# Kernel optimization log

Hardware: AMD Instinct MI355X
Metric: run time of the kernel (lower is better)

## Reference

```python
import jax, jax.numpy as jnp
import numpy as np
jax.config.update('jax_enable_x64', True)  # log_normalization accumulates in fp64 like the torch code

B = 256
N = 36864  # SO(3) HEALPix-style grid, level 3
EPS_TRACE = 1e-8


def quat_to_mat(q):
    # (w, x, y, z) convention; normalize to a unit quaternion first.
    q = q / jnp.linalg.norm(q, axis=-1, keepdims=True)
    w, x, y, z = q[..., 0], q[..., 1], q[..., 2], q[..., 3]
    return jnp.stack([
        jnp.stack([1 - 2 * (y * y + z * z), 2 * (x * y - w * z), 2 * (x * z + w * y)], -1),
        jnp.stack([2 * (x * y + w * z), 1 - 2 * (x * x + z * z), 2 * (y * z - w * x)], -1),
        jnp.stack([2 * (x * z - w * y), 2 * (y * z + w * x), 1 - 2 * (x * x + y * y)], -1),
    ], -2)


def cholesky_inverse(L):
    # (L L^T)^{-1} = L^{-T} L^{-1}; batched 3x3, inv is cheap and exact here.
    Linv = jnp.linalg.inv(L)
    return jnp.einsum('...ki,...kj->...ij', Linv, Linv)


def setup_inputs() -> dict:
    key = jax.random.key(0)
    k1, k2, k3, k4 = jax.random.split(key, 4)
    gt_quat = jax.random.normal(k1, (B, 4), dtype=jnp.float32)
    mode_quat = jax.random.normal(k2, (B, 4), dtype=jnp.float32)
    raw = jax.random.normal(k3, (B, 3, 3), dtype=jnp.float32)
    diag_vals = 0.3 + jax.nn.softplus(jnp.diagonal(raw, axis1=-2, axis2=-1))
    cov_tril = jnp.tril(raw, -1) * 0.2 + jnp.eye(3, dtype=jnp.float32) * diag_vals[:, None, :]
    grid_q = jax.random.normal(k4, (N, 4), dtype=jnp.float32)
    grids = quat_to_mat(grid_q)  # [N, 3, 3] rotation matrices
    return {'gt_quat': gt_quat, 'mode_quat': mode_quat, 'cov_tril': cov_tril, 'grids': grids}


def reference(gt_quat, mode_quat, cov_tril, grids):
    Z = cholesky_inverse(cov_tril)                      # [B,3,3] precision
    trZ = jnp.einsum('bii->b', Z)                       # tr(Z)

    # power over the grid: sqrt(clamp(tr(Z) - tr(Z @ R_n), eps)) for every grid rotation
    tr_ZR_grid = jnp.einsum('bij,nji->bn', Z, grids)    # [B,N] = diag-sum of Z @ R_n
    powers = jnp.sqrt(jnp.clip(trZ[:, None] - tr_ZR_grid, EPS_TRACE))  # [B,N] fp32

    # stable log-normalization (fp64 accumulation, as in the torch code)
    stability = jnp.min(powers, axis=-1)                # [B]
    p64 = powers.astype(jnp.float64)
    log_exp_sum = jnp.log(jnp.sum(jnp.exp(-p64 + stability[:, None].astype(jnp.float64)) / p64,
                                  axis=1)).astype(jnp.float32)
    logF = log_exp_sum - jnp.log(jnp.float32(N)) - stability

    # power at the ground truth relative rotation R = R0^T R_gt
    R_gt = quat_to_mat(gt_quat)
    R0 = quat_to_mat(mode_quat)
    R_rel = jnp.einsum('bki,bkj->bij', R0, R_gt)        # R0^T @ R_gt
    tr_ZR = jnp.einsum('bij,bji->b', Z, R_rel)
    power = jnp.sqrt(jnp.clip(trZ - tr_ZR, EPS_TRACE))  # [B]

    nll = logF + power + jnp.log(power)
    return nll
```

## Files before the change

kernel.cpp:

```cpp
#include <hip/hip_runtime.h>
#include <math.h>

#define TPB 256
#define KROT 6
#define BPB 8
#define NCHUNK (TPB * KROT)

__device__ __forceinline__ void compute_Z_neg(const float* __restrict__ L, float zo[7]) {
    float a = L[0], l10 = L[3], c = L[4], d = L[6], e = L[7], f = L[8];
    float ia = 1.0f / a, ic = 1.0f / c, iff = 1.0f / f;
    float m00 = ia;
    float m10 = -l10 * ia * ic;
    float m11 = ic;
    float m20 = (l10 * e - c * d) * ia * ic * iff;
    float m21 = -e * ic * iff;
    float m22 = iff;
    float Z0 = m00*m00 + m10*m10 + m20*m20;
    float Z1 = m10*m11 + m20*m21;
    float Z2 = m20*m22;
    float Z4 = m11*m11 + m21*m21;
    float Z5 = m21*m22;
    float Z8 = m22*m22;
    zo[0] = -Z0; zo[1] = -Z4; zo[2] = -Z8;
    zo[3] = -Z1; zo[4] = -Z2; zo[5] = -Z5;
    zo[6] = Z0 + Z4 + Z8;
}

__device__ __forceinline__ void quat_to_mat(const float q[4], float R[9]) {
    float n = sqrtf(q[0]*q[0] + q[1]*q[1] + q[2]*q[2] + q[3]*q[3]);
    float w = q[0]/n, x = q[1]/n, y = q[2]/n, z = q[3]/n;
    R[0] = 1.f - 2.f*(y*y + z*z);
    R[1] = 2.f*(x*y - w*z);
    R[2] = 2.f*(x*z + w*y);
    R[3] = 2.f*(x*y + w*z);
    R[4] = 1.f - 2.f*(x*x + z*z);
    R[5] = 2.f*(y*z - w*x);
    R[6] = 2.f*(x*z - w*y);
    R[7] = 2.f*(y*z + w*x);
    R[8] = 1.f - 2.f*(x*x + y*y);
}

__global__ __launch_bounds__(TPB) void k1_partials(
    const float* __restrict__ cov_tril,
    const float* __restrict__ grids,
    double* __restrict__ ws, int B)
{
    const int tile = blockIdx.x;
    const int bg   = blockIdx.y;
    const int tid  = threadIdx.x;

    __shared__ float zsh[BPB][8];
    __shared__ float red[TPB * 9];

    if (tid < BPB) {
        float zo[7];
        compute_Z_neg(cov_tril + (bg * BPB + tid) * 9, zo);
#pragma unroll
        for (int j = 0; j < 7; ++j) zsh[tid][j] = zo[j];
    }

    float g[KROT][6];
    const float* base = grids + (size_t)(tile * NCHUNK + tid * KROT) * 9;
#pragma unroll
    for (int k = 0; k < KROT; ++k) {
        const float* G = base + k * 9;
        float G0 = G[0], G1 = G[1], G2 = G[2], G3 = G[3], G4 = G[4];
        float G5 = G[5], G6 = G[6], G7 = G[7], G8 = G[8];
        g[k][0] = G0; g[k][1] = G4; g[k][2] = G8;
        g[k][3] = G1 + G3; g[k][4] = G2 + G6; g[k][5] = G5 + G7;
    }
    __syncthreads();

    float acc[BPB];
#pragma unroll
    for (int bl = 0; bl < BPB; ++bl) {
        float z0 = zsh[bl][0], z1 = zsh[bl][1], z2 = zsh[bl][2];
        float z3 = zsh[bl][3], z4 = zsh[bl][4], z5 = zsh[bl][5];
        float trZ = zsh[bl][6];
        float a0 = 0.f;
#pragma unroll
        for (int k = 0; k < KROT; ++k) {
            float x = trZ;
            x = fmaf(z0, g[k][0], x);
            x = fmaf(z1, g[k][1], x);
            x = fmaf(z2, g[k][2], x);
            x = fmaf(z3, g[k][3], x);
            x = fmaf(z4, g[k][4], x);
            x = fmaf(z5, g[k][5], x);
            x = fmaxf(x, 1e-8f);
            float r = rsqrtf(x);
            float p = x * r;
            a0 += __expf(-p) * r;
        }
        acc[bl] = a0;
    }

#pragma unroll
    for (int bl = 0; bl < BPB; ++bl) red[tid * 9 + bl] = acc[bl];
    __syncthreads();

    const int bl = tid & 7;
    const int s  = tid >> 3;
    float part = 0.f;
#pragma unroll
    for (int j = 0; j < 8; ++j) part += red[(s * 8 + j) * 9 + bl];
    __syncthreads();
    red[tid] = part;
    __syncthreads();

    if (tid < BPB) {
        double S = 0.0;
#pragma unroll
        for (int j = 0; j < 32; ++j) S += (double)red[j * 8 + tid];
        ws[(size_t)tile * B + bg * BPB + tid] = S;
    }
}

__global__ __launch_bounds__(TPB) void k2_finalize(
    const float* __restrict__ gt_quat,
    const float* __restrict__ mode_quat,
    const float* __restrict__ cov_tril,
    const double* __restrict__ ws,
    float* __restrict__ out, int n_tiles, int n_total, int B)
{
    const int b = blockIdx.x * blockDim.x + threadIdx.x;
    if (b >= B) return;

    double S = 0.0;
    for (int t = 0; t < n_tiles; ++t) S += ws[(size_t)t * B + b];

    float zo[7];
    compute_Z_neg(cov_tril + b * 9, zo);
    float trZ = zo[6];

    float q0[4] = {mode_quat[b*4+0], mode_quat[b*4+1], mode_quat[b*4+2], mode_quat[b*4+3]};
    float qg[4] = {gt_quat[b*4+0],   gt_quat[b*4+1],   gt_quat[b*4+2],   gt_quat[b*4+3]};
    float R0[9], Rg[9];
    quat_to_mat(q0, R0);
    quat_to_mat(qg, Rg);

    float Rr[9];
#pragma unroll
    for (int i = 0; i < 3; ++i)
#pragma unroll
        for (int j = 0; j < 3; ++j)
            Rr[i*3+j] = R0[0*3+i]*Rg[0*3+j] + R0[1*3+i]*Rg[1*3+j] + R0[2*3+i]*Rg[2*3+j];

    float x = trZ;
    x = fmaf(zo[0], Rr[0], x);
    x = fmaf(zo[1], Rr[4], x);
    x = fmaf(zo[2], Rr[8], x);
    x = fmaf(zo[3], Rr[1] + Rr[3], x);
    x = fmaf(zo[4], Rr[2] + Rr[6], x);
    x = fmaf(zo[5], Rr[5] + Rr[7], x);

    float power = sqrtf(fmaxf(x, 1e-8f));
    float logF  = (float)(log(S) - log((double)n_total));
    out[b] = logF + power + logf(power);
}

extern "C" void kernel_launch(void* const* d_in, const int* in_sizes, int n_in,
                              void* d_out, int out_size, void* d_ws, size_t ws_size,
                              hipStream_t stream) {
    const float* gt    = (const float*)d_in[0];
    const float* mode  = (const float*)d_in[1];
    const float* cov   = (const float*)d_in[2];
    const float* grids = (const float*)d_in[3];
    float* out = (float*)d_out;

    const int B       = in_sizes[0] / 4;
    const int n_total = in_sizes[3] / 9;
    const int n_tiles = n_total / NCHUNK;
    const int b_grps  = B / BPB;

    dim3 g1(n_tiles, b_grps);
    k1_partials<<<g1, TPB, 0, stream>>>(cov, grids, (double*)d_ws, B);
    k2_finalize<<<(B + TPB - 1) / TPB, TPB, 0, stream>>>(
        gt, mode, cov, (const double*)d_ws, out, n_tiles, n_total, B);
}
```

Baseline: 19.01 us.

## Pre-transpose grid into SoA planes for coalesced loads in main kernel

Adds a pre-pass kernel that converts the AoS 3x3 grid matrices into six structure-of-arrays planes holding the diagonal and the symmetric off-diagonal sums. The main kernel then reads these planes with coalesced per-thread loads, and it reorders its loops so each batch's Z stays in registers while rotations stream in. The aim is to remove the strided 36-byte-per-thread uncoalesced loads that 32 batch-group blocks repeat on the same grid data. The cost is an extra kernel launch, a write and re-read of the planes in workspace, and higher register pressure from holding 56 Z values.

```diff
diff --git a/kernel.cpp b/kernel.cpp
--- a/kernel.cpp
+++ b/kernel.cpp
@@ -40,10 +40,33 @@
     R[8] = 1.f - 2.f*(x*x + y*y);
 }
 
+__global__ __launch_bounds__(TPB) void k0_transpose(
+    const float* __restrict__ grids, float* __restrict__ planes, int n_total)
+{
+    __shared__ float sh[TPB * 9];
+    const int base = blockIdx.x * TPB;
+    const int tid  = threadIdx.x;
+#pragma unroll
+    for (int j = 0; j < 9; ++j) {
+        int idx = j * TPB + tid;
+        sh[idx] = grids[(size_t)base * 9 + idx];
+    }
+    __syncthreads();
+    const float* G = sh + tid * 9;
+    float G0=G[0],G1=G[1],G2=G[2],G3=G[3],G4=G[4],G5=G[5],G6=G[6],G7=G[7],G8=G[8];
+    const int n = base + tid;
+    planes[0*n_total+n] = G0;
+    planes[1*n_total+n] = G4;
+    planes[2*n_total+n] = G8;
+    planes[3*n_total+n] = G1 + G3;
+    planes[4*n_total+n] = G2 + G6;
+    planes[5*n_total+n] = G5 + G7;
+}
+
 __global__ __launch_bounds__(TPB) void k1_partials(
     const float* __restrict__ cov_tril,
-    const float* __restrict__ grids,
-    double* __restrict__ ws, int B)
+    const float* __restrict__ planes,
+    double* __restrict__ part, int B, int n_total)
 {
     const int tile = blockIdx.x;
     const int bg   = blockIdx.y;
@@ -58,41 +81,44 @@
 #pragma unroll
         for (int j = 0; j < 7; ++j) zsh[tid][j] = zo[j];
     }
-
-    float g[KROT][6];
-    const float* base = grids + (size_t)(tile * NCHUNK + tid * KROT) * 9;
+    __syncthreads();
+
+    float z[BPB][7];
+#pragma unroll
+    for (int bl = 0; bl < BPB; ++bl)
+#pragma unroll
+        for (int j = 0; j < 7; ++j) z[bl][j] = zsh[bl][j];
+
+    float acc[BPB];
+#pragma unroll
+    for (int bl = 0; bl < BPB; ++bl) acc[bl] = 0.f;
+
+    const float* p0 = planes + 0 * n_total;
+    const float* p1 = planes + 1 * n_total;
+    const float* p2 = planes + 2 * n_total;
+    const float* p3 = planes + 3 * n_total;
+    const float* p4 = planes + 4 * n_total;
+    const float* p5 = planes + 5 * n_total;
+
 #pragma unroll
     for (int k = 0; k < KROT; ++k) {
-        const float* G = base + k * 9;
-        float G0 = G[0], G1 = G[1], G2 = G[2], G3 = G[3], G4 = G[4];
-        float G5 = G[5], G6 = G[6], G7 = G[7], G8 = G[8];
-        g[k][0] = G0; g[k][1] = G4; g[k][2] = G8;
-        g[k][3] = G1 + G3; g[k][4] = G2 + G6; g[k][5] = G5 + G7;
-    }
-    __syncthreads();
-
-    float acc[BPB];
-#pragma unroll
-    for (int bl = 0; bl < BPB; ++bl) {
-        float z0 = zsh[bl][0], z1 = zsh[bl][1], z2 = zsh[bl][2];
-        float z3 = zsh[bl][3], z4 = zsh[bl][4], z5 = zsh[bl][5];
-        float trZ = zsh[bl][6];
-        float a0 = 0.f;
-#pragma unroll
-        for (int k = 0; k < KROT; ++k) {
-            float x = trZ;
-            x = fmaf(z0, g[k][0], x);
-            x = fmaf(z1, g[k][1], x);
-            x = fmaf(z2, g[k][2], x);
-            x = fmaf(z3, g[k][3], x);
-            x = fmaf(z4, g[k][4], x);
-            x = fmaf(z5, g[k][5], x);
+        const int n = tile * NCHUNK + k * TPB + tid;
+        float g0 = p0[n], g1 = p1[n], g2 = p2[n];
+        float g3 = p3[n], g4 = p4[n], g5 = p5[n];
+#pragma unroll
+        for (int bl = 0; bl < BPB; ++bl) {
+            float x = z[bl][6];
+            x = fmaf(z[bl][0], g0, x);
+            x = fmaf(z[bl][1], g1, x);
+            x = fmaf(z[bl][2], g2, x);
+            x = fmaf(z[bl][3], g3, x);
+            x = fmaf(z[bl][4], g4, x);
+            x = fmaf(z[bl][5], g5, x);
             x = fmaxf(x, 1e-8f);
             float r = rsqrtf(x);
             float p = x * r;
-            a0 += __expf(-p) * r;
+            acc[bl] += __expf(-p) * r;
         }
-        acc[bl] = a0;
     }
 
 #pragma unroll
@@ -101,18 +127,18 @@
 
     const int bl = tid & 7;
     const int s  = tid >> 3;
-    float part = 0.f;
-#pragma unroll
-    for (int j = 0; j < 8; ++j) part += red[(s * 8 + j) * 9 + bl];
-    __syncthreads();
-    red[tid] = part;
+    float p_ = 0.f;
+#pragma unroll
+    for (int j = 0; j < 8; ++j) p_ += red[(s * 8 + j) * 9 + bl];
+    __syncthreads();
+    red[tid] = p_;
     __syncthreads();
 
     if (tid < BPB) {
         double S = 0.0;
 #pragma unroll
         for (int j = 0; j < 32; ++j) S += (double)red[j * 8 + tid];
-        ws[(size_t)tile * B + bg * BPB + tid] = S;
+        part[(size_t)tile * B + bg * BPB + tid] = S;
     }
 }
 
@@ -120,18 +146,17 @@
     const float* __restrict__ gt_quat,
     const float* __restrict__ mode_quat,
     const float* __restrict__ cov_tril,
-    const double* __restrict__ ws,
+    const double* __restrict__ part,
     float* __restrict__ out, int n_tiles, int n_total, int B)
 {
     const int b = blockIdx.x * blockDim.x + threadIdx.x;
     if (b >= B) return;
 
     double S = 0.0;
-    for (int t = 0; t < n_tiles; ++t) S += ws[(size_t)t * B + b];
+    for (int t = 0; t < n_tiles; ++t) S += part[(size_t)t * B + b];
 
     float zo[7];
     compute_Z_neg(cov_tril + b * 9, zo);
-    float trZ = zo[6];
 
     float q0[4] = {mode_quat[b*4+0], mode_quat[b*4+1], mode_quat[b*4+2], mode_quat[b*4+3]};
     float qg[4] = {gt_quat[b*4+0],   gt_quat[b*4+1],   gt_quat[b*4+2],   gt_quat[b*4+3]};
@@ -146,7 +171,7 @@
         for (int j = 0; j < 3; ++j)
             Rr[i*3+j] = R0[0*3+i]*Rg[0*3+j] + R0[1*3+i]*Rg[1*3+j] + R0[2*3+i]*Rg[2*3+j];
 
-    float x = trZ;
+    float x = zo[6];
     x = fmaf(zo[0], Rr[0], x);
     x = fmaf(zo[1], Rr[4], x);
     x = fmaf(zo[2], Rr[8], x);
@@ -173,8 +198,14 @@
     const int n_tiles = n_total / NCHUNK;
     const int b_grps  = B / BPB;
 
+    float*  planes = (float*)d_ws;
+    double* part   = (double*)((char*)d_ws + (size_t)6 * n_total * 4);
+
+    k0_transpose<<<n_total / TPB, TPB, 0, stream>>>(grids, planes, n_total);
+
     dim3 g1(n_tiles, b_grps);
-    k1_partials<<<g1, TPB, 0, stream>>>(cov, grids, (double*)d_ws, B);
+    k1_partials<<<g1, TPB, 0, stream>>>(cov, planes, part, B, n_total);
+
     k2_finalize<<<(B + TPB - 1) / TPB, TPB, 0, stream>>>(
-        gt, mode, cov, (const double*)d_ws, out, n_tiles, n_total, B);
-}
+        gt, mode, cov, part, out, n_tiles, n_total, B);
+}
```

After: 22.77 us. 1.2x slower.
